# Kernel tuning notes

Measured on AMD Instinct MI355X. Metric: run time of the kernel, lower is better.

## Reference

```python
import jax, jax.numpy as jnp
import numpy as np
import math

D_MODEL = 2048
N_HEADS = 16
BATCH = 2
SEQ = 2048
ALIBI_BIAS_MAX = 8


def alibi_bias(n_heads, seq_len, alibi_bias_max=8):
    # matches torch alibi_bias(full=False): shape [1, n_heads, 1, seq_len]
    dist = jnp.arange(1 - seq_len, 1, dtype=jnp.float32).reshape(1, 1, 1, seq_len)
    m = jnp.arange(1, n_heads + 1, dtype=jnp.float32) * (alibi_bias_max / n_heads)
    slopes = 1.0 / (2.0 ** m).reshape(1, n_heads, 1, 1)
    return dist * slopes


def setup_inputs() -> dict:
    key = jax.random.key(0)
    ks = jax.random.split(key, 5)
    d = D_MODEL
    scale = 1.0 / math.sqrt(d)
    x = jax.random.normal(ks[0], (BATCH, SEQ, d), dtype=jnp.float32)
    w_qkv = jax.random.normal(ks[1], (3 * d, d), dtype=jnp.float32) * scale
    b_qkv = jnp.zeros((3 * d,), dtype=jnp.float32)
    w_out = jax.random.normal(ks[2], (d, d), dtype=jnp.float32) * scale
    b_out = jnp.zeros((d,), dtype=jnp.float32)
    attn_mask = alibi_bias(N_HEADS, SEQ, ALIBI_BIAS_MAX)
    return {"x": x, "attn_mask": attn_mask, "w_qkv": w_qkv, "b_qkv": b_qkv,
            "w_out": w_out, "b_out": b_out}


def reference(x, attn_mask, w_qkv, b_qkv, w_out, b_out):
    B, S, D = x.shape
    H = N_HEADS
    hd = D // H
    # packed QKV projection
    qkv = x @ w_qkv.T + b_qkv                      # [B,S,3D]
    qkv = qkv.reshape(B, S, 3, H, hd)
    q, k, v = qkv[:, :, 0], qkv[:, :, 1], qkv[:, :, 2]  # [B,S,H,hd]
    scores = jnp.einsum('bqhd,bkhd->bhqk', q, k) * (1.0 / math.sqrt(hd))
    scores = scores + attn_mask                    # ALiBi additive bias [1,H,1,S]
    causal = jnp.tril(jnp.ones((S, S), dtype=bool))
    scores = jnp.where(causal, scores, -jnp.inf)
    probs = jax.nn.softmax(scores, axis=-1)        # [B,H,S,S]
    ctx = jnp.einsum('bhqk,bkhd->bqhd', probs, v).reshape(B, S, D)
    return ctx @ w_out.T + b_out
```

## Files before the change

kernel.cpp:

```cpp
#include <hip/hip_runtime.h>
#include <math.h>

typedef unsigned short u16;
typedef __attribute__((ext_vector_type(8))) short short8;
typedef __attribute__((ext_vector_type(4))) float f32x4;

#define MFMA16x16x32(a, b, c) __builtin_amdgcn_mfma_f32_16x16x32_bf16((a), (b), (c), 0, 0, 0)
#define GLL16(g, s)                                                        \
  __builtin_amdgcn_global_load_lds(                                        \
      (const __attribute__((address_space(1))) void*)(g),                  \
      (__attribute__((address_space(3))) void*)(s), 16, 0, 0)

__device__ __forceinline__ u16 f32_to_bf16(float x) {
  union { float f; unsigned u; } v; v.f = x;
  unsigned r = v.u + 0x7FFFu + ((v.u >> 16) & 1u);
  return (u16)(r >> 16);
}

__global__ void cvt_f32_bf16(const float* __restrict__ in, u16* __restrict__ out, int n4) {
  int i = blockIdx.x * blockDim.x + threadIdx.x;
  int stride = gridDim.x * blockDim.x;
  for (; i < n4; i += stride) {
    float4 v = ((const float4*)in)[i];
    ushort4 o;
    o.x = f32_to_bf16(v.x);
    o.y = f32_to_bf16(v.y);
    o.z = f32_to_bf16(v.z);
    o.w = f32_to_bf16(v.w);
    ((ushort4*)out)[i] = o;
  }
}

template <int OUT_BF16>
__global__ __launch_bounds__(512, 2) void gemm_nt_p2(
    const u16* __restrict__ A,
    const u16* __restrict__ B,
    const float* __restrict__ bias,
    void* __restrict__ C,
    int M, int N, int K)
{
  __shared__ u16 As[2][8192];
  __shared__ u16 Bs[3][16384];

  const int tid = threadIdx.x;
  const int w = tid >> 6, l = tid & 63;
  const int l15 = l & 15, l4 = l >> 4;
  const int wm = w >> 2, wn = w & 3;
  const long bm = (long)blockIdx.y * 128, bn = (long)blockIdx.x * 256;
  const int NT = K >> 6;

  const u16 *aSrc0, *aSrc1, *bSrc0, *bSrc1;
  {
    int q = w * 2048 + l * 16;
    int r = q >> 7, cb = (q & 127) ^ ((r & 7) << 4);
    aSrc0 = A + (bm + r) * (long)K + (cb >> 1);
    bSrc0 = B + (bn + r) * (long)K + (cb >> 1);
    q += 1024;
    r = q >> 7; cb = (q & 127) ^ ((r & 7) << 4);
    aSrc1 = A + (bm + r) * (long)K + (cb >> 1);
    bSrc1 = B + (bn + r) * (long)K + (cb >> 1);
  }
  const long bHS = 128 * (long)K;
  const int ldst = w * 1024;

#define STAGE6(tt)                                                            \
  do {                                                                        \
    const long ko = (long)(tt) * 64;                                          \
    const int vb = (tt) % 3, ab = (tt) & 1;                                   \
    GLL16(aSrc0 + ko, &As[ab][ldst]);                                         \
    GLL16(aSrc1 + ko, &As[ab][ldst + 512]);                                   \
    GLL16(bSrc0 + ko, &Bs[vb][ldst]);                                         \
    GLL16(bSrc1 + ko, &Bs[vb][ldst + 512]);                                   \
    GLL16(bSrc0 + bHS + ko, &Bs[vb][8192 + ldst]);                            \
    GLL16(bSrc1 + bHS + ko, &Bs[vb][8192 + ldst + 512]);                      \
  } while (0)

  const f32x4 z4 = {0.f, 0.f, 0.f, 0.f};
  f32x4 acc[4][4];
  #pragma unroll
  for (int m = 0; m < 4; ++m)
    #pragma unroll
    for (int n = 0; n < 4; ++n) acc[m][n] = z4;

  const int xo0 = (l4 * 16) ^ ((l15 & 7) << 4);
  const int xo1 = (64 + l4 * 16) ^ ((l15 & 7) << 4);

  short8 af[4][2], bf[4][2];

  STAGE6(0);
  STAGE6(1);
  asm volatile("s_waitcnt vmcnt(6)\ns_barrier" ::: "memory");

  for (int t = 0; t < NT; ++t) {
    const char* ab = (const char*)&As[t & 1][0] + (wm * 64 + l15) * 128;
    const char* bb = (const char*)&Bs[t % 3][0] + (wn * 32 + l15) * 128;

    #pragma unroll
    for (int m = 0; m < 4; ++m) {
      af[m][0] = *(const short8*)(ab + m * 2048 + xo0);
      af[m][1] = *(const short8*)(ab + m * 2048 + xo1);
    }
    #pragma unroll
    for (int n = 0; n < 2; ++n) {
      bf[n][0] = *(const short8*)(bb + n * 2048 + xo0);
      bf[n][1] = *(const short8*)(bb + n * 2048 + xo1);
    }
    asm volatile("s_waitcnt lgkmcnt(0)" ::: "memory");
    __builtin_amdgcn_s_setprio(1);
    #pragma unroll
    for (int m = 0; m < 4; ++m)
      #pragma unroll
      for (int n = 0; n < 2; ++n) {
        acc[m][n] = MFMA16x16x32(af[m][0], bf[n][0], acc[m][n]);
        acc[m][n] = MFMA16x16x32(af[m][1], bf[n][1], acc[m][n]);
      }
    __builtin_amdgcn_s_setprio(0);
    asm volatile("s_barrier" ::: "memory");

    #pragma unroll
    for (int n = 0; n < 2; ++n) {
      bf[2 + n][0] = *(const short8*)(bb + 16384 + n * 2048 + xo0);
      bf[2 + n][1] = *(const short8*)(bb + 16384 + n * 2048 + xo1);
    }
    if (t + 2 < NT) STAGE6(t + 2);
    if (t >= NT - 2)
      asm volatile("s_waitcnt vmcnt(0) lgkmcnt(0)" ::: "memory");
    else
      asm volatile("s_waitcnt vmcnt(6) lgkmcnt(0)" ::: "memory");
    __builtin_amdgcn_s_setprio(1);
    #pragma unroll
    for (int m = 0; m < 4; ++m)
      #pragma unroll
      for (int n = 2; n < 4; ++n) {
        acc[m][n] = MFMA16x16x32(af[m][0], bf[n][0], acc[m][n]);
        acc[m][n] = MFMA16x16x32(af[m][1], bf[n][1], acc[m][n]);
      }
    __builtin_amdgcn_s_setprio(0);
    asm volatile("s_barrier" ::: "memory");
  }
#undef STAGE6

  #pragma unroll
  for (int m = 0; m < 4; ++m) {
    const long row0 = bm + wm * 64 + m * 16 + l4 * 4;
    #pragma unroll
    for (int n = 0; n < 4; ++n) {
      const long col = bn + wn * 32 + (n & 1) * 16 + (n >> 1) * 128 + l15;
      const float bv = bias[col];
      #pragma unroll
      for (int r = 0; r < 4; ++r) {
        const float v = acc[m][n][r] + bv;
        if (OUT_BF16)
          ((u16*)C)[(row0 + r) * (long)N + col] = f32_to_bf16(v);
        else
          ((float*)C)[(row0 + r) * (long)N + col] = v;
      }
    }
  }
}

__global__ __launch_bounds__(256) void repack_kv(
    const u16* __restrict__ qkv, u16* __restrict__ kimg, u16* __restrict__ vimg)
{
  const int t = blockIdx.x;
  const int h = blockIdx.y, b = blockIdx.z;
  const int tid = threadIdx.x;
  __shared__ u16 Vl[64][136];

  const long qbase = ((long)(b * 2048 + t * 64)) * 6144 + h * 128;
  u16* kout = kimg + (((long)(b * 16 + h) * 32 + t) * 8192);
  u16* vout = vimg + (((long)(b * 16 + h) * 32 + t) * 8192);

  #pragma unroll
  for (int i = 0; i < 4; ++i) {
    const int j = tid + i * 256;
    {
      const int r = j >> 4, c8 = (j & 15) * 8;
      uint4 v = *(const uint4*)(qkv + qbase + (long)r * 6144 + 4096 + c8);
      *(uint4*)(&Vl[r][c8]) = v;
    }
    {
      const int byte = j * 16;
      const int r = byte >> 8;
      const int wv = (byte & 255) ^ ((r & 7) << 4);
      const int d0 = wv >> 1;
      uint4 v = *(const uint4*)(qkv + qbase + (long)r * 6144 + 2048 + d0);
      *(uint4*)(kout + j * 8) = v;
    }
  }
  __syncthreads();
  #pragma unroll
  for (int i = 0; i < 4; ++i) {
    const int j = tid + i * 256;
    const int byte = j * 16;
    const int d = byte >> 7;
    const int wv = (byte & 127) ^ ((d & 7) << 4);
    const int k0 = wv >> 1;
    u16 tmp[8];
    #pragma unroll
    for (int m = 0; m < 8; ++m) tmp[m] = Vl[k0 + m][d];
    *(uint4*)(vout + j * 8) = *(const uint4*)tmp;
  }
}

__global__ __launch_bounds__(256) void attn_kernel(
    const u16* __restrict__ qkv,
    const u16* __restrict__ kimg,
    const u16* __restrict__ vimg,
    u16* __restrict__ ctx)
{
  const int S = 2048, NHD = 6144, NT = 32;
  const int p = blockIdx.x, h = blockIdx.y, b = blockIdx.z;
  const int tid = threadIdx.x;
  const int w = tid >> 6, l = tid & 63;
  const int l15 = l & 15, l4 = l >> 4;

  __shared__ u16 Ks[64 * 128];
  __shared__ u16 Vt[128 * 64];
  __shared__ u16 Ps[4][16 * 64];

  const float LOG2E = 1.44269504088896f;
  const float c1 = 0.08838834764831845f * LOG2E;
  const float slope2 = exp2f(-0.5f * (float)(h + 1)) * LOG2E;

  const f32x4 z4 = {0.f, 0.f, 0.f, 0.f};

  for (int pass = 0; pass < 2; ++pass) {
    const int qblk = pass ? (NT - 1 - p) : p;
    const int qb0 = qblk * 64;

    short8 qf[4];
    {
      const int qrow = qb0 + w * 16 + l15;
      const u16* qp = qkv + (long)(b * S + qrow) * NHD + h * 128 + l4 * 8;
      #pragma unroll
      for (int kc = 0; kc < 4; ++kc) qf[kc] = *(const short8*)(qp + kc * 32);
    }

    f32x4 o[8];
    #pragma unroll
    for (int i = 0; i < 8; ++i) o[i] = z4;
    float m_r[4] = {-3.0e38f, -3.0e38f, -3.0e38f, -3.0e38f};
    float l_r[4] = {0.f, 0.f, 0.f, 0.f};

    for (int kt = 0; kt <= qblk; ++kt) {
      const u16* ksrc = kimg + (((long)(b * 16 + h) * NT + kt) * 8192);
      const u16* vsrc = vimg + (((long)(b * 16 + h) * NT + kt) * 8192);
      #pragma unroll
      for (int i = 0; i < 4; ++i) {
        const int chunk = w * 4 + i;
        __builtin_amdgcn_global_load_lds(
            (const __attribute__((address_space(1))) void*)(ksrc + chunk * 512 + l * 8),
            (__attribute__((address_space(3))) void*)(Ks + chunk * 512), 16, 0, 0);
        __builtin_amdgcn_global_load_lds(
            (const __attribute__((address_space(1))) void*)(vsrc + chunk * 512 + l * 8),
            (__attribute__((address_space(3))) void*)(Vt + chunk * 512), 16, 0, 0);
      }
      __syncthreads();

      f32x4 sf[4];
      #pragma unroll
      for (int nt = 0; nt < 4; ++nt) sf[nt] = z4;
      #pragma unroll
      for (int nt = 0; nt < 4; ++nt) {
        const int krow = nt * 16 + l15;
        #pragma unroll
        for (int kc = 0; kc < 4; ++kc) {
          int kbyte = (krow * 256 + kc * 64 + l4 * 16) ^ ((krow & 7) << 4);
          const short8 kf = *(const short8*)((const char*)Ks + kbyte);
          sf[nt] = MFMA16x16x32(qf[kc], kf, sf[nt]);
        }
      }

      float add_nt[4];
      int kg_nt[4];
      #pragma unroll
      for (int nt = 0; nt < 4; ++nt) {
        kg_nt[nt] = kt * 64 + nt * 16 + l15;
        add_nt[nt] = slope2 * (float)(kg_nt[nt] - (S - 1));
      }
      const bool diag = (kt == qblk);
      float alpha[4];
      #pragma unroll
      for (int r = 0; r < 4; ++r) {
        const int qrow_l = l4 * 4 + r;
        const int qg = qb0 + w * 16 + qrow_l;
        float sc[4];
        #pragma unroll
        for (int nt = 0; nt < 4; ++nt) sc[nt] = sf[nt][r] * c1 + add_nt[nt];
        if (diag) {
          #pragma unroll
          for (int nt = 0; nt < 4; ++nt)
            if (kg_nt[nt] > qg) sc[nt] = -3.0e38f;
        }
        float mx = fmaxf(fmaxf(sc[0], sc[1]), fmaxf(sc[2], sc[3]));
        #pragma unroll
        for (int d = 1; d < 16; d <<= 1) mx = fmaxf(mx, __shfl_xor(mx, d, 64));
        const float mnew = fmaxf(m_r[r], mx);
        float sum = 0.f;
        #pragma unroll
        for (int nt = 0; nt < 4; ++nt) {
          const float pv = exp2f(sc[nt] - mnew);
          sc[nt] = pv;
          sum += pv;
        }
        #pragma unroll
        for (int d = 1; d < 16; d <<= 1) sum += __shfl_xor(sum, d, 64);
        alpha[r] = exp2f(m_r[r] - mnew);
        l_r[r] = l_r[r] * alpha[r] + sum;
        m_r[r] = mnew;
        #pragma unroll
        for (int nt = 0; nt < 4; ++nt) {
          int pbyte = ((qrow_l * 64 + nt * 16 + l15) * 2) ^ ((qrow_l & 7) << 4);
          *(u16*)((char*)&Ps[w][0] + pbyte) = f32_to_bf16(sc[nt]);
        }
      }

      #pragma unroll
      for (int nt = 0; nt < 8; ++nt)
        #pragma unroll
        for (int r = 0; r < 4; ++r) o[nt][r] *= alpha[r];

      #pragma unroll
      for (int kc = 0; kc < 2; ++kc) {
        int pbyte = ((l15 * 64 + kc * 32 + l4 * 8) * 2) ^ ((l15 & 7) << 4);
        const short8 pf = *(const short8*)((const char*)&Ps[w][0] + pbyte);
        #pragma unroll
        for (int nt = 0; nt < 8; ++nt) {
          const int d = nt * 16 + l15;
          const int vbyte = ((d * 128 + kc * 64 + l4 * 16)) ^ ((d & 7) << 4);
          const short8 vf = *(const short8*)((const char*)Vt + vbyte);
          o[nt] = MFMA16x16x32(pf, vf, o[nt]);
        }
      }
      __syncthreads();
    }

    float rl[4];
    #pragma unroll
    for (int r = 0; r < 4; ++r) rl[r] = 1.0f / l_r[r];
    #pragma unroll
    for (int nt = 0; nt < 8; ++nt) {
      #pragma unroll
      for (int r = 0; r < 4; ++r) {
        const int qg = qb0 + w * 16 + l4 * 4 + r;
        ctx[(long)(b * S + qg) * 2048 + h * 128 + nt * 16 + l15] =
            f32_to_bf16(o[nt][r] * rl[r]);
      }
    }
  }
}

extern "C" void kernel_launch(void* const* d_in, const int* in_sizes, int n_in,
                              void* d_out, int out_size, void* d_ws, size_t ws_size,
                              hipStream_t stream) {
  const float* x     = (const float*)d_in[0];
  const float* w_qkv = (const float*)d_in[2];
  const float* b_qkv = (const float*)d_in[3];
  const float* w_out = (const float*)d_in[4];
  const float* b_out = (const float*)d_in[5];
  float* out = (float*)d_out;

  char* ws = (char*)d_ws;
  u16* xb    = (u16*)(ws);
  u16* wqkvb = (u16*)(ws + 16777216UL);
  u16* woutb = (u16*)(ws + 41943040UL);
  u16* qkvb  = (u16*)(ws + 50331648UL);
  u16* ctxb  = (u16*)(ws + 100663296UL);
  u16* kimg  = (u16*)(ws);
  u16* vimg  = (u16*)(ws + 16777216UL);

  cvt_f32_bf16<<<2048, 256, 0, stream>>>(x, xb, 8388608 / 4);
  cvt_f32_bf16<<<2048, 256, 0, stream>>>(w_qkv, wqkvb, 12582912 / 4);
  cvt_f32_bf16<<<2048, 256, 0, stream>>>(w_out, woutb, 4194304 / 4);

  gemm_nt_p2<1><<<dim3(24, 32), 512, 0, stream>>>(xb, wqkvb, b_qkv, (void*)qkvb, 4096, 6144, 2048);

  repack_kv<<<dim3(32, 16, 2), 256, 0, stream>>>(qkvb, kimg, vimg);

  attn_kernel<<<dim3(16, 16, 2), 256, 0, stream>>>(qkvb, kimg, vimg, ctxb);

  gemm_nt_p2<0><<<dim3(8, 32), 512, 0, stream>>>(ctxb, woutb, b_out, (void*)out, 4096, 2048, 2048);
}
```

Baseline: 307.3 us.

## Double-buffer K/V tiles in attention with 128-row query blocks and fuse conversions

The attention kernel now uses 512 threads (8 waves) per 128-row query block. K/V tiles are double-buffered in LDS, and the next tile is prefetched while the current one is computed, so load latency is hidden behind MFMA work. Softmax max/sum reductions are interleaved across the four rows to expose more ILP, and the causal mask is applied on every tile instead of only the diagonal. The three f32→bf16 conversion launches are merged into one kernel. The grid halves to 256 blocks, which risks lower occupancy, and LDS use per block grows.

```diff
diff --git a/kernel.cpp b/kernel.cpp
--- a/kernel.cpp
+++ b/kernel.cpp
@@ -17,18 +17,24 @@
   return (u16)(r >> 16);
 }
 
-__global__ void cvt_f32_bf16(const float* __restrict__ in, u16* __restrict__ out, int n4) {
-  int i = blockIdx.x * blockDim.x + threadIdx.x;
-  int stride = gridDim.x * blockDim.x;
-  for (; i < n4; i += stride) {
-    float4 v = ((const float4*)in)[i];
-    ushort4 o;
-    o.x = f32_to_bf16(v.x);
-    o.y = f32_to_bf16(v.y);
-    o.z = f32_to_bf16(v.z);
-    o.w = f32_to_bf16(v.w);
-    ((ushort4*)out)[i] = o;
-  }
+__device__ __forceinline__ void cvt4(const float* in, u16* out, int j) {
+  float4 v = ((const float4*)in)[j];
+  ushort4 o;
+  o.x = f32_to_bf16(v.x);
+  o.y = f32_to_bf16(v.y);
+  o.z = f32_to_bf16(v.z);
+  o.w = f32_to_bf16(v.w);
+  ((ushort4*)out)[j] = o;
+}
+
+__global__ void cvt_all(const float* __restrict__ x, const float* __restrict__ wq,
+                        const float* __restrict__ wo, u16* __restrict__ xb,
+                        u16* __restrict__ wqb, u16* __restrict__ wob) {
+  const int stride = gridDim.x * blockDim.x;
+  const int i = blockIdx.x * blockDim.x + threadIdx.x;
+  for (int j = i; j < 2097152; j += stride) cvt4(x, xb, j);
+  for (int j = i; j < 3145728; j += stride) cvt4(wq, wqb, j);
+  for (int j = i; j < 1048576; j += stride) cvt4(wo, wob, j);
 }
 
 template <int OUT_BF16>
@@ -203,31 +209,48 @@
   }
 }
 
-__global__ __launch_bounds__(256) void attn_kernel(
+__global__ __launch_bounds__(512) void attn_kernel(
     const u16* __restrict__ qkv,
     const u16* __restrict__ kimg,
     const u16* __restrict__ vimg,
     u16* __restrict__ ctx)
 {
-  const int S = 2048, NHD = 6144, NT = 32;
+  const int S = 2048, NHD = 6144;
   const int p = blockIdx.x, h = blockIdx.y, b = blockIdx.z;
   const int tid = threadIdx.x;
   const int w = tid >> 6, l = tid & 63;
   const int l15 = l & 15, l4 = l >> 4;
 
-  __shared__ u16 Ks[64 * 128];
-  __shared__ u16 Vt[128 * 64];
-  __shared__ u16 Ps[4][16 * 64];
+  __shared__ u16 Kd[2][8192];
+  __shared__ u16 Vd[2][8192];
+  __shared__ u16 Ps[8][1024];
 
   const float LOG2E = 1.44269504088896f;
   const float c1 = 0.08838834764831845f * LOG2E;
   const float slope2 = exp2f(-0.5f * (float)(h + 1)) * LOG2E;
 
+  const long ibase = ((long)(b * 16 + h) * 32) * 8192;
+  const u16* kbase = kimg + ibase;
+  const u16* vbase = vimg + ibase;
+
+#define ASTAGE(kt, buf)                                                       \
+  do {                                                                        \
+    const u16* _ks = kbase + (long)(kt) * 8192;                               \
+    const u16* _vs = vbase + (long)(kt) * 8192;                               \
+    _Pragma("unroll")                                                         \
+    for (int _i = 0; _i < 2; ++_i) {                                          \
+      const int _c = w * 2 + _i;                                              \
+      GLL16(_ks + _c * 512 + l * 8, &Kd[buf][_c * 512]);                      \
+      GLL16(_vs + _c * 512 + l * 8, &Vd[buf][_c * 512]);                      \
+    }                                                                         \
+  } while (0)
+
   const f32x4 z4 = {0.f, 0.f, 0.f, 0.f};
 
   for (int pass = 0; pass < 2; ++pass) {
-    const int qblk = pass ? (NT - 1 - p) : p;
-    const int qb0 = qblk * 64;
+    const int Q = pass ? (15 - p) : p;
+    const int qb0 = Q * 128;
+    const int NTkv = 2 * Q + 2;
 
     short8 qf[4];
     {
@@ -243,20 +266,14 @@
     float m_r[4] = {-3.0e38f, -3.0e38f, -3.0e38f, -3.0e38f};
     float l_r[4] = {0.f, 0.f, 0.f, 0.f};
 
-    for (int kt = 0; kt <= qblk; ++kt) {
-      const u16* ksrc = kimg + (((long)(b * 16 + h) * NT + kt) * 8192);
-      const u16* vsrc = vimg + (((long)(b * 16 + h) * NT + kt) * 8192);
-      #pragma unroll
-      for (int i = 0; i < 4; ++i) {
-        const int chunk = w * 4 + i;
-        __builtin_amdgcn_global_load_lds(
-            (const __attribute__((address_space(1))) void*)(ksrc + chunk * 512 + l * 8),
-            (__attribute__((address_space(3))) void*)(Ks + chunk * 512), 16, 0, 0);
-        __builtin_amdgcn_global_load_lds(
-            (const __attribute__((address_space(1))) void*)(vsrc + chunk * 512 + l * 8),
-            (__attribute__((address_space(3))) void*)(Vt + chunk * 512), 16, 0, 0);
-      }
-      __syncthreads();
+    ASTAGE(0, 0);
+    __syncthreads();
+
+    for (int kt = 0; kt < NTkv; ++kt) {
+      if (kt + 1 < NTkv) ASTAGE(kt + 1, (kt + 1) & 1);
+      const int cb = kt & 1;
+      const char* Kc = (const char*)&Kd[cb][0];
+      const char* Vc = (const char*)&Vd[cb][0];
 
       f32x4 sf[4];
       #pragma unroll
@@ -267,7 +284,7 @@
         #pragma unroll
         for (int kc = 0; kc < 4; ++kc) {
           int kbyte = (krow * 256 + kc * 64 + l4 * 16) ^ ((krow & 7) << 4);
-          const short8 kf = *(const short8*)((const char*)Ks + kbyte);
+          const short8 kf = *(const short8*)(Kc + kbyte);
           sf[nt] = MFMA16x16x32(qf[kc], kf, sf[nt]);
         }
       }
@@ -279,40 +296,53 @@
         kg_nt[nt] = kt * 64 + nt * 16 + l15;
         add_nt[nt] = slope2 * (float)(kg_nt[nt] - (S - 1));
       }
-      const bool diag = (kt == qblk);
-      float alpha[4];
+      float sc[4][4], mxv[4];
+      #pragma unroll
+      for (int r = 0; r < 4; ++r) {
+        const int qg = qb0 + w * 16 + l4 * 4 + r;
+        #pragma unroll
+        for (int nt = 0; nt < 4; ++nt) {
+          float s = sf[nt][r] * c1 + add_nt[nt];
+          if (kg_nt[nt] > qg) s = -3.0e38f;
+          sc[r][nt] = s;
+        }
+        mxv[r] = fmaxf(fmaxf(sc[r][0], sc[r][1]), fmaxf(sc[r][2], sc[r][3]));
+      }
+      #pragma unroll
+      for (int d = 1; d < 16; d <<= 1) {
+        #pragma unroll
+        for (int r = 0; r < 4; ++r)
+          mxv[r] = fmaxf(mxv[r], __shfl_xor(mxv[r], d, 64));
+      }
+      float alpha[4], sum[4];
+      #pragma unroll
+      for (int r = 0; r < 4; ++r) {
+        const float mnew = fmaxf(m_r[r], mxv[r]);
+        sum[r] = 0.f;
+        #pragma unroll
+        for (int nt = 0; nt < 4; ++nt) {
+          const float pv = exp2f(sc[r][nt] - mnew);
+          sc[r][nt] = pv;
+          sum[r] += pv;
+        }
+        alpha[r] = exp2f(m_r[r] - mnew);
+        m_r[r] = mnew;
+      }
+      #pragma unroll
+      for (int d = 1; d < 16; d <<= 1) {
+        #pragma unroll
+        for (int r = 0; r < 4; ++r) sum[r] += __shfl_xor(sum[r], d, 64);
+      }
+      #pragma unroll
+      for (int r = 0; r < 4; ++r) l_r[r] = l_r[r] * alpha[r] + sum[r];
+
       #pragma unroll
       for (int r = 0; r < 4; ++r) {
         const int qrow_l = l4 * 4 + r;
-        const int qg = qb0 + w * 16 + qrow_l;
-        float sc[4];
-        #pragma unroll
-        for (int nt = 0; nt < 4; ++nt) sc[nt] = sf[nt][r] * c1 + add_nt[nt];
-        if (diag) {
-          #pragma unroll
-          for (int nt = 0; nt < 4; ++nt)
-            if (kg_nt[nt] > qg) sc[nt] = -3.0e38f;
-        }
-        float mx = fmaxf(fmaxf(sc[0], sc[1]), fmaxf(sc[2], sc[3]));
-        #pragma unroll
-        for (int d = 1; d < 16; d <<= 1) mx = fmaxf(mx, __shfl_xor(mx, d, 64));
-        const float mnew = fmaxf(m_r[r], mx);
-        float sum = 0.f;
-        #pragma unroll
-        for (int nt = 0; nt < 4; ++nt) {
-          const float pv = exp2f(sc[nt] - mnew);
-          sc[nt] = pv;
-          sum += pv;
-        }
-        #pragma unroll
-        for (int d = 1; d < 16; d <<= 1) sum += __shfl_xor(sum, d, 64);
-        alpha[r] = exp2f(m_r[r] - mnew);
-        l_r[r] = l_r[r] * alpha[r] + sum;
-        m_r[r] = mnew;
         #pragma unroll
         for (int nt = 0; nt < 4; ++nt) {
           int pbyte = ((qrow_l * 64 + nt * 16 + l15) * 2) ^ ((qrow_l & 7) << 4);
-          *(u16*)((char*)&Ps[w][0] + pbyte) = f32_to_bf16(sc[nt]);
+          *(u16*)((char*)&Ps[w][0] + pbyte) = f32_to_bf16(sc[r][nt]);
         }
       }
 
@@ -329,7 +359,7 @@
         for (int nt = 0; nt < 8; ++nt) {
           const int d = nt * 16 + l15;
           const int vbyte = ((d * 128 + kc * 64 + l4 * 16)) ^ ((d & 7) << 4);
-          const short8 vf = *(const short8*)((const char*)Vt + vbyte);
+          const short8 vf = *(const short8*)(Vc + vbyte);
           o[nt] = MFMA16x16x32(pf, vf, o[nt]);
         }
       }
@@ -348,7 +378,9 @@
             f32_to_bf16(o[nt][r] * rl[r]);
       }
     }
-  }
+    __syncthreads();
+  }
+#undef ASTAGE
 }
 
 extern "C" void kernel_launch(void* const* d_in, const int* in_sizes, int n_in,
@@ -370,15 +402,13 @@
   u16* kimg  = (u16*)(ws);
   u16* vimg  = (u16*)(ws + 16777216UL);
 
-  cvt_f32_bf16<<<2048, 256, 0, stream>>>(x, xb, 8388608 / 4);
-  cvt_f32_bf16<<<2048, 256, 0, stream>>>(w_qkv, wqkvb, 12582912 / 4);
-  cvt_f32_bf16<<<2048, 256, 0, stream>>>(w_out, woutb, 4194304 / 4);
+  cvt_all<<<2048, 256, 0, stream>>>(x, w_qkv, w_out, xb, wqkvb, woutb);
 
   gemm_nt_p2<1><<<dim3(24, 32), 512, 0, stream>>>(xb, wqkvb, b_qkv, (void*)qkvb, 4096, 6144, 2048);
 
   repack_kv<<<dim3(32, 16, 2), 256, 0, stream>>>(qkvb, kimg, vimg);
 
-  attn_kernel<<<dim3(16, 16, 2), 256, 0, stream>>>(qkvb, kimg, vimg, ctxb);
+  attn_kernel<<<dim3(8, 16, 2), 512, 0, stream>>>(qkvb, kimg, vimg, ctxb);
 
   gemm_nt_p2<0><<<dim3(8, 32), 512, 0, stream>>>(ctxb, woutb, b_out, (void*)out, 4096, 2048, 2048);
 }
```

After: 293.7 us. -4.4%, faster.
